# Kernel optimization log

Hardware: AMD Instinct MI355X
Metric: run time of the kernel (lower is better)

## Reference

```python
import jax, jax.numpy as jnp
import numpy as np

SCALE = 1.0 / np.sqrt(64.0)  # module hardcodes 64**0.5, independent of d


def setup_inputs() -> dict:
    key = jax.random.key(0)
    k1, k2 = jax.random.split(key)
    x = jax.random.normal(k1, (8, 2048, 512), dtype=jnp.float32)
    kernel = jax.random.normal(k2, (3, 512, 512), dtype=jnp.float32) * 0.02
    return {"x": x, "kernel": kernel}


def reference(x, kernel):
    # x: [b, s, d]; kernel: [3, d, d]
    q = jnp.einsum('bsd,de->bse', x, kernel[0])
    k = jnp.einsum('bsd,de->bse', x, kernel[1])
    v = jnp.einsum('bsd,de->bse', x, kernel[2])
    scores = jnp.einsum('bqd,bkd->bqk', q, k) * SCALE  # [b, s, s]
    attn = jax.nn.softmax(scores, axis=-1)
    return jnp.einsum('bqk,bkd->bqd', attn, v)
```

## Files before the change

kernel.cpp:

```cpp
#include <hip/hip_runtime.h>


typedef unsigned short u16;
typedef unsigned int u32;

using bf16x8 = __attribute__((ext_vector_type(8))) short;
using f32x4  = __attribute__((ext_vector_type(4))) float;
using u16x4  = __attribute__((ext_vector_type(4))) u16;

__device__ __forceinline__ u16 f2bf(float f) {
  u32 u = __float_as_uint(f);
  u32 r = (u + 0x7FFFu + ((u >> 16) & 1u)) >> 16;
  return (u16)r;
}
__device__ __forceinline__ float bf2f(u16 h) {
  return __uint_as_float(((u32)h) << 16);
}

#define GLL16(src, dst)                                                        \
  __builtin_amdgcn_global_load_lds(                                            \
      (const __attribute__((address_space(1))) void*)(src),                    \
      (__attribute__((address_space(3))) void*)(dst), 16, 0, 0)

template <int K, bool RSUM>
__device__ __forceinline__ void gemm8p_256x128(
    const u16* __restrict__ A0, const u16* __restrict__ B0,
    u16* lds, f32x4 (&acc)[4][4], float* rs)
{
  const int tid = threadIdx.x;
  const int w = tid >> 6, l = tid & 63;
  const int wm = w >> 1, wn = w & 1;
  const int fr = l & 15;
  const int laneChunk = ((l >> 4) ^ ((fr >> 1) & 3)) << 3;
  const int laneA = (wm * 64 + fr) * 32 + laneChunk;
  const int laneB = (wn * 64 + fr) * 32 + laneChunk;
  u16* const ldsA = lds;
  u16* const ldsB = lds + 24576;

  const int chunkS = ((tid & 3) ^ ((tid >> 3) & 3)) << 3;
  const int r0 = tid >> 2;
  const u16* const sA0 = A0 + (size_t)r0 * K + chunkS;
  const u16* const sA1 = A0 + (size_t)(r0 + 128) * K + chunkS;
  const u16* const sB0 = B0 + (size_t)r0 * K + chunkS;
  const int dOf = w * 512;

#define PSTAGE_A(j, slot) do {                                                 \
    u16* d_ = ldsA + (slot) * 8192 + dOf;                                      \
    GLL16(sA0 + (j) * 32, d_);                                                 \
    GLL16(sA1 + (j) * 32, d_ + 4096);                                          \
  } while (0)
#define PSTAGE_B(j, slot) do {                                                 \
    u16* d_ = ldsB + (slot) * 4096 + dOf;                                      \
    GLL16(sB0 + (j) * 32, d_);                                                 \
  } while (0)

  PSTAGE_B(0, 0); PSTAGE_A(0, 0);
  PSTAGE_B(1, 1); PSTAGE_A(1, 1);

  constexpr int NS = K / 32;
  int slot = 0;
  for (int j = 0; j < NS; ++j) {
    const int jn = (j + 2 < NS) ? (j + 2) : (NS - 1);
    int slotn = slot + 2; if (slotn >= 3) slotn -= 3;

    asm volatile("s_waitcnt vmcnt(3)\n\ts_barrier" ::: "memory");

    const u16* const Ab = ldsA + slot * 8192;
    const u16* const Bb = ldsB + slot * 4096;
    bf16x8 a[4], b[4];
#pragma unroll
    for (int i = 0; i < 4; ++i) a[i] = *(const bf16x8*)(Ab + laneA + i * 512);
#pragma unroll
    for (int i = 0; i < 4; ++i) b[i] = *(const bf16x8*)(Bb + laneB + i * 512);
    PSTAGE_B(jn, slotn);
    __builtin_amdgcn_s_setprio(1);
#pragma unroll
    for (int mi = 0; mi < 2; ++mi)
#pragma unroll
      for (int nj = 0; nj < 4; ++nj)
        acc[mi][nj] = __builtin_amdgcn_mfma_f32_16x16x32_bf16(a[mi], b[nj], acc[mi][nj], 0, 0, 0);
    __builtin_amdgcn_s_setprio(0);
    PSTAGE_A(jn, slotn);
    __builtin_amdgcn_s_setprio(1);
#pragma unroll
    for (int mi = 2; mi < 4; ++mi)
#pragma unroll
      for (int nj = 0; nj < 4; ++nj)
        acc[mi][nj] = __builtin_amdgcn_mfma_f32_16x16x32_bf16(a[mi], b[nj], acc[mi][nj], 0, 0, 0);
    __builtin_amdgcn_s_setprio(0);

    if (RSUM) {
#pragma unroll
      for (int i = 0; i < 4; ++i) {
        float s_ = 0.f;
#pragma unroll
        for (int e = 0; e < 8; ++e) s_ += bf2f((u16)a[i][e]);
        rs[i] += s_;
      }
    }

    slot = (slot == 2) ? 0 : slot + 1;
  }
#undef PSTAGE_A
#undef PSTAGE_B
}

template <int K>
__device__ __forceinline__ void gemm8p_256sq_pp(
    const u16* __restrict__ A0, const u16* __restrict__ B0,
    u16* lds, f32x4 (&acc)[8][4])
{
  const int tid = threadIdx.x;
  const int w = tid >> 6, l = tid & 63;
  const int wm = w >> 2, wn = w & 3;
  const int fr = l & 15;
  const int laneChunk = ((l >> 4) ^ ((fr >> 1) & 3)) << 3;
  const int laneA = (wm * 128 + fr) * 32 + laneChunk;
  const int laneB = (wn * 64 + fr) * 32 + laneChunk;
  u16* const ldsA = lds;
  u16* const ldsB = lds + 24576;

  const int chunkS = ((tid & 3) ^ ((tid >> 3) & 3)) << 3;
  const int r0 = tid >> 2;
  const u16* const sA0 = A0 + (size_t)r0 * K + chunkS;
  const u16* const sA1 = A0 + (size_t)(r0 + 128) * K + chunkS;
  const u16* const sB0 = B0 + (size_t)r0 * K + chunkS;
  const u16* const sB1 = B0 + (size_t)(r0 + 128) * K + chunkS;
  const int dOf = w * 512;

#define SSTAGE_A(j, slot) do {                                                 \
    u16* d_ = ldsA + (slot) * 8192 + dOf;                                      \
    GLL16(sA0 + (j) * 32, d_);                                                 \
    GLL16(sA1 + (j) * 32, d_ + 4096);                                          \
  } while (0)
#define SSTAGE_B(j, slot) do {                                                 \
    u16* d_ = ldsB + (slot) * 8192 + dOf;                                      \
    GLL16(sB0 + (j) * 32, d_);                                                 \
    GLL16(sB1 + (j) * 32, d_ + 4096);                                          \
  } while (0)

  constexpr int NS = K / 32;
  bf16x8 bP[4], aP0[4], aP1[4], bQ[4], aQ0[4], aQ1[4];

  SSTAGE_B(0, 0); SSTAGE_A(0, 0);
  SSTAGE_B(1, 1); SSTAGE_A(1, 1);
  SSTAGE_B(2, 2); SSTAGE_A(2, 2);
  asm volatile("s_waitcnt vmcnt(8)\n\ts_barrier" ::: "memory");
#pragma unroll
  for (int i = 0; i < 4; ++i) bP[i]  = *(const bf16x8*)(ldsB + laneB + i * 512);
#pragma unroll
  for (int i = 0; i < 4; ++i) aP0[i] = *(const bf16x8*)(ldsA + laneA + i * 512);
#pragma unroll
  for (int i = 0; i < 4; ++i) aP1[i] = *(const bf16x8*)(ldsA + laneA + (4 + i) * 512);

#define SITER(jj, CB, CA0, CA1, NB, NA0, NA1) do {                             \
    const int js_ = ((jj) + 3 < NS) ? (jj) + 3 : NS - 1;                       \
    const int sS_ = (jj) % 3;                                                  \
    const int sR_ = ((jj) + 1) % 3;                                            \
    asm volatile("s_waitcnt vmcnt(4) lgkmcnt(0)\n\ts_barrier" ::: "memory");   \
    const u16* const Ab_ = ldsA + sR_ * 8192;                                  \
    const u16* const Bb_ = ldsB + sR_ * 8192;                                  \
    _Pragma("unroll")                                                          \
    for (int i = 0; i < 4; ++i) NB[i]  = *(const bf16x8*)(Bb_ + laneB + i * 512); \
    _Pragma("unroll")                                                          \
    for (int i = 0; i < 4; ++i) NA0[i] = *(const bf16x8*)(Ab_ + laneA + i * 512); \
    SSTAGE_A(js_, sS_);                                                        \
    __builtin_amdgcn_s_setprio(1);                                             \
    _Pragma("unroll")                                                          \
    for (int mi = 0; mi < 4; ++mi)                                             \
      _Pragma("unroll")                                                        \
      for (int nj = 0; nj < 4; ++nj)                                           \
        acc[mi][nj] = __builtin_amdgcn_mfma_f32_16x16x32_bf16(                 \
            CA0[mi], CB[nj], acc[mi][nj], 0, 0, 0);                            \
    __builtin_amdgcn_s_setprio(0);                                             \
    _Pragma("unroll")                                                          \
    for (int i = 0; i < 4; ++i) NA1[i] = *(const bf16x8*)(Ab_ + laneA + (4 + i) * 512); \
    SSTAGE_B(js_, sS_);                                                        \
    __builtin_amdgcn_s_setprio(1);                                             \
    _Pragma("unroll")                                                          \
    for (int mi = 0; mi < 4; ++mi)                                             \
      _Pragma("unroll")                                                        \
      for (int nj = 0; nj < 4; ++nj)                                           \
        acc[4 + mi][nj] = __builtin_amdgcn_mfma_f32_16x16x32_bf16(             \
            CA1[mi], CB[nj], acc[4 + mi][nj], 0, 0, 0);                        \
    __builtin_amdgcn_s_setprio(0);                                             \
  } while (0)

  for (int j = 0; j < NS; j += 2) {
    SITER(j, bP, aP0, aP1, bQ, aQ0, aQ1);
    SITER(j + 1, bQ, aQ0, aQ1, bP, aP0, aP1);
  }
#undef SITER
#undef SSTAGE_A
#undef SSTAGE_B
}


__global__ void convert_x_kernel(const float* __restrict__ x, u16* __restrict__ xb) {
  int i = blockIdx.x * 256 + threadIdx.x;
  float4 f = ((const float4*)x)[i];
  u16x4 o = { f2bf(f.x), f2bf(f.y), f2bf(f.z), f2bf(f.w) };
  ((u16x4*)xb)[i] = o;
}

__global__ void convw_kernel(const float* __restrict__ W, u16* __restrict__ wT) {
  __shared__ float tile[32][33];
  const int mtx = blockIdx.z;
  const int e0 = blockIdx.x * 32, d0 = blockIdx.y * 32;
  const int tx = threadIdx.x, ty = threadIdx.y;
  const float* Wm = W + (size_t)mtx * 262144;
#pragma unroll
  for (int i = 0; i < 32; i += 8)
    tile[ty + i][tx] = Wm[(size_t)(d0 + ty + i) * 512 + e0 + tx];
  __syncthreads();
  u16* T = wT + (size_t)mtx * 262144;
#pragma unroll
  for (int i = 0; i < 32; i += 8)
    T[(size_t)(e0 + ty + i) * 512 + d0 + tx] = f2bf(tile[tx][ty + i]);
}

__global__ __launch_bounds__(512, 4) void gemm_qkv128_kernel(
    const u16* __restrict__ xb, const u16* __restrict__ wT,
    u16* __restrict__ qb, u16* __restrict__ kb, u16* __restrict__ vt)
{
  __shared__ __align__(16) u16 lds[36864];
  const int id = blockIdx.x;
  const int xcd = id & 7, t = id >> 3;
  const int n0 = (t % 12) * 128;
  const int m0 = (xcd * 8 + t / 12) * 256;
  f32x4 acc[4][4] = {};
  gemm8p_256x128<512, false>(xb + (size_t)m0 * 512, wT + (size_t)n0 * 512, lds, acc, nullptr);

  const int tid = threadIdx.x, w = tid >> 6, l = tid & 63;
  const int wm = w >> 1, wn = w & 1;
  const int which = n0 >> 9;
  const int eb = (n0 & 511) + wn * 64 + (l & 15);
  const int rb = m0 + wm * 64 + (l >> 4) * 4;
  if (which < 2) {
    u16* dst = which ? kb : qb;
#pragma unroll
    for (int mi = 0; mi < 4; ++mi)
#pragma unroll
      for (int nj = 0; nj < 4; ++nj) {
        const int row = rb + mi * 16;
        const int col = eb + nj * 16;
#pragma unroll
        for (int r = 0; r < 4; ++r)
          dst[(size_t)(row + r) * 512 + col] = f2bf(acc[mi][nj][r]);
      }
  } else {
#pragma unroll
    for (int mi = 0; mi < 4; ++mi)
#pragma unroll
      for (int nj = 0; nj < 4; ++nj) {
        const int s = rb + mi * 16;
        const int b = s >> 11, sl = s & 2047;
        const int e = eb + nj * 16;
        u16x4 pk;
#pragma unroll
        for (int r = 0; r < 4; ++r) pk[r] = f2bf(acc[mi][nj][r]);
        *(u16x4*)(vt + (size_t)b * 1048576 + (size_t)e * 2048 + sl) = pk;
      }
  }
}

__global__ __launch_bounds__(512, 2) void gemm_scores256_kernel(
    const u16* __restrict__ qb, const u16* __restrict__ kb, u16* __restrict__ attn)
{
  __shared__ __align__(16) u16 lds[49152];
  const int id = blockIdx.x;
  const int z = id & 7, t = id >> 3;
  const int n0 = (t & 7) * 256;
  const int m0 = (t >> 3) * 256;
  f32x4 acc[8][4] = {};
  gemm8p_256sq_pp<512>(qb + (size_t)z * 1048576 + (size_t)m0 * 512,
                       kb + (size_t)z * 1048576 + (size_t)n0 * 512, lds, acc);

  const int tid = threadIdx.x, w = tid >> 6, l = tid & 63;
  const int wm = w >> 2, wn = w & 3;
  u16* C = attn + (size_t)z * 4194304;
  const int rb = m0 + wm * 128 + (l >> 4) * 4;
  const int cb = n0 + wn * 64 + (l & 15);
#pragma unroll
  for (int mi = 0; mi < 8; ++mi)
#pragma unroll
    for (int nj = 0; nj < 4; ++nj) {
      const int row = rb + mi * 16;
      const int col = cb + nj * 16;
#pragma unroll
      for (int r = 0; r < 4; ++r)
        C[(size_t)(row + r) * 2048 + col] = f2bf(__expf(acc[mi][nj][r] * 0.125f));
    }
}

__global__ __launch_bounds__(512, 4) void gemm_pv8p_kernel(
    const u16* __restrict__ attn, const u16* __restrict__ vt, float* __restrict__ out)
{
  __shared__ __align__(16) u16 lds[36864];
  __shared__ float rowsumLDS[256];
  const int id = blockIdx.x;
  const int z = id & 7;
  const int j = id >> 3;
  const int n0 = (j & 3) * 128;
  const int m0 = (j >> 2) * 256;
  f32x4 acc[4][4] = {};
  float rs[4] = {0.f, 0.f, 0.f, 0.f};
  gemm8p_256x128<2048, true>(attn + (size_t)z * 4194304 + (size_t)m0 * 2048,
                             vt + (size_t)z * 1048576 + (size_t)n0 * 2048, lds, acc, rs);

  const int tid = threadIdx.x, w = tid >> 6, l = tid & 63;
  const int wm = w >> 1, wn = w & 1;

  __syncthreads();
#pragma unroll
  for (int mi = 0; mi < 4; ++mi) {
    rs[mi] += __shfl_xor(rs[mi], 16);
    rs[mi] += __shfl_xor(rs[mi], 32);
  }
  if ((l >> 4) == 0) {
#pragma unroll
    for (int mi = 0; mi < 4; ++mi)
      rowsumLDS[wm * 64 + mi * 16 + l] = rs[mi];
  }
  __syncthreads();

  float* C = out + (size_t)z * 1048576;
  const int rb = m0 + wm * 64 + (l >> 4) * 4;
  const int cb = n0 + wn * 64 + (l & 15);
#pragma unroll
  for (int mi = 0; mi < 4; ++mi)
#pragma unroll
    for (int r = 0; r < 4; ++r) {
      const float inv = 1.f / rowsumLDS[wm * 64 + mi * 16 + (l >> 4) * 4 + r];
      const int row = rb + mi * 16 + r;
#pragma unroll
      for (int nj = 0; nj < 4; ++nj)
        C[(size_t)row * 512 + cb + nj * 16] = acc[mi][nj][r] * inv;
    }
}

extern "C" void kernel_launch(void* const* d_in, const int* in_sizes, int n_in,
                              void* d_out, int out_size, void* d_ws, size_t ws_size,
                              hipStream_t stream) {
  const float* x = (const float*)d_in[0];
  const float* W = (const float*)d_in[1];
  float* out = (float*)d_out;

  if (ws_size < 117440512) return;
  u16* wsu  = (u16*)d_ws;
  u16* qb   = wsu;
  u16* kb   = qb + 8388608;
  u16* vt   = kb + 8388608;
  u16* attn = vt + 8388608;
  u16* xb   = attn;
  u16* wT   = attn + 8388608;

  convert_x_kernel<<<8192, 256, 0, stream>>>(x, xb);
  convw_kernel<<<dim3(16, 16, 3), dim3(32, 8), 0, stream>>>(W, wT);
  gemm_qkv128_kernel<<<768, 512, 0, stream>>>(xb, wT, qb, kb, vt);
  gemm_scores256_kernel<<<512, 512, 0, stream>>>(qb, kb, attn);
  gemm_pv8p_kernel<<<256, 512, 0, stream>>>(attn, vt, out);
}
```

Before: 132.0 us.

## Register double-buffer GEMM fragments and move softmax rowsum into scores epilogue

The 256x128 GEMM core now prefetches the next k-step's LDS fragments into a second register set while MFMAs run on the current one, with three stages of global loads in flight. When the workspace is large enough, the scores kernel accumulates exp row sums in fp32 and atomically adds them to a global buffer, which convert_x zeroes beforehand. The PV kernel then reads these sums instead of re-summing bf16 attention fragments. This removes per-iteration rowsum ALU work in PV, at the cost of atomics in the scores epilogue, more register pressure, and a fast path that only runs if the workspace exceeds the prior size.

```diff
diff --git a/kernel.cpp b/kernel.cpp
--- a/kernel.cpp
+++ b/kernel.cpp
@@ -23,7 +23,7 @@
       (__attribute__((address_space(3))) void*)(dst), 16, 0, 0)
 
 template <int K, bool RSUM>
-__device__ __forceinline__ void gemm8p_256x128(
+__device__ __forceinline__ void gemm128_pp(
     const u16* __restrict__ A0, const u16* __restrict__ B0,
     u16* lds, f32x4 (&acc)[4][4], float* rs)
 {
@@ -54,53 +54,63 @@
     GLL16(sB0 + (j) * 32, d_);                                                 \
   } while (0)
 
+  constexpr int NS = K / 32;
+  bf16x8 aP[4], bP[4], aQ[4], bQ[4];
+
   PSTAGE_B(0, 0); PSTAGE_A(0, 0);
   PSTAGE_B(1, 1); PSTAGE_A(1, 1);
-
-  constexpr int NS = K / 32;
-  int slot = 0;
-  for (int j = 0; j < NS; ++j) {
-    const int jn = (j + 2 < NS) ? (j + 2) : (NS - 1);
-    int slotn = slot + 2; if (slotn >= 3) slotn -= 3;
-
-    asm volatile("s_waitcnt vmcnt(3)\n\ts_barrier" ::: "memory");
-
-    const u16* const Ab = ldsA + slot * 8192;
-    const u16* const Bb = ldsB + slot * 4096;
-    bf16x8 a[4], b[4];
-#pragma unroll
-    for (int i = 0; i < 4; ++i) a[i] = *(const bf16x8*)(Ab + laneA + i * 512);
-#pragma unroll
-    for (int i = 0; i < 4; ++i) b[i] = *(const bf16x8*)(Bb + laneB + i * 512);
-    PSTAGE_B(jn, slotn);
-    __builtin_amdgcn_s_setprio(1);
-#pragma unroll
-    for (int mi = 0; mi < 2; ++mi)
-#pragma unroll
-      for (int nj = 0; nj < 4; ++nj)
-        acc[mi][nj] = __builtin_amdgcn_mfma_f32_16x16x32_bf16(a[mi], b[nj], acc[mi][nj], 0, 0, 0);
-    __builtin_amdgcn_s_setprio(0);
-    PSTAGE_A(jn, slotn);
-    __builtin_amdgcn_s_setprio(1);
-#pragma unroll
-    for (int mi = 2; mi < 4; ++mi)
-#pragma unroll
-      for (int nj = 0; nj < 4; ++nj)
-        acc[mi][nj] = __builtin_amdgcn_mfma_f32_16x16x32_bf16(a[mi], b[nj], acc[mi][nj], 0, 0, 0);
-    __builtin_amdgcn_s_setprio(0);
-
-    if (RSUM) {
-#pragma unroll
-      for (int i = 0; i < 4; ++i) {
-        float s_ = 0.f;
-#pragma unroll
-        for (int e = 0; e < 8; ++e) s_ += bf2f((u16)a[i][e]);
-        rs[i] += s_;
-      }
-    }
-
-    slot = (slot == 2) ? 0 : slot + 1;
+  PSTAGE_B(2, 2); PSTAGE_A(2, 2);
+  asm volatile("s_waitcnt vmcnt(6)\n\ts_barrier" ::: "memory");
+#pragma unroll
+  for (int i = 0; i < 4; ++i) aP[i] = *(const bf16x8*)(ldsA + laneA + i * 512);
+#pragma unroll
+  for (int i = 0; i < 4; ++i) bP[i] = *(const bf16x8*)(ldsB + laneB + i * 512);
+
+#define KITER(jj, CA, CB, NA, NB) do {                                         \
+    const int js_ = ((jj) + 3 < NS) ? (jj) + 3 : NS - 1;                       \
+    const int sS_ = (jj) % 3;                                                  \
+    const int sR_ = ((jj) + 1) % 3;                                            \
+    asm volatile("s_waitcnt vmcnt(3) lgkmcnt(0)\n\ts_barrier" ::: "memory");   \
+    const u16* const Ab_ = ldsA + sR_ * 8192;                                  \
+    const u16* const Bb_ = ldsB + sR_ * 4096;                                  \
+    _Pragma("unroll")                                                          \
+    for (int i = 0; i < 4; ++i) NB[i] = *(const bf16x8*)(Bb_ + laneB + i * 512); \
+    _Pragma("unroll")                                                          \
+    for (int i = 0; i < 4; ++i) NA[i] = *(const bf16x8*)(Ab_ + laneA + i * 512); \
+    PSTAGE_B(js_, sS_);                                                        \
+    __builtin_amdgcn_s_setprio(1);                                             \
+    _Pragma("unroll")                                                          \
+    for (int mi = 0; mi < 2; ++mi)                                             \
+      _Pragma("unroll")                                                        \
+      for (int nj = 0; nj < 4; ++nj)                                           \
+        acc[mi][nj] = __builtin_amdgcn_mfma_f32_16x16x32_bf16(                 \
+            CA[mi], CB[nj], acc[mi][nj], 0, 0, 0);                             \
+    __builtin_amdgcn_s_setprio(0);                                             \
+    PSTAGE_A(js_, sS_);                                                        \
+    __builtin_amdgcn_s_setprio(1);                                             \
+    _Pragma("unroll")                                                          \
+    for (int mi = 2; mi < 4; ++mi)                                             \
+      _Pragma("unroll")                                                        \
+      for (int nj = 0; nj < 4; ++nj)                                           \
+        acc[mi][nj] = __builtin_amdgcn_mfma_f32_16x16x32_bf16(                 \
+            CA[mi], CB[nj], acc[mi][nj], 0, 0, 0);                             \
+    __builtin_amdgcn_s_setprio(0);                                             \
+    if (RSUM) {                                                                \
+      _Pragma("unroll")                                                        \
+      for (int i = 0; i < 4; ++i) {                                            \
+        float s_ = 0.f;                                                        \
+        _Pragma("unroll")                                                      \
+        for (int e = 0; e < 8; ++e) s_ += bf2f((u16)CA[i][e]);                 \
+        rs[i] += s_;                                                           \
+      }                                                                        \
+    }                                                                          \
+  } while (0)
+
+  for (int j = 0; j < NS; j += 2) {
+    KITER(j, aP, bP, aQ, bQ);
+    KITER(j + 1, aQ, bQ, aP, bP);
   }
+#undef KITER
 #undef PSTAGE_A
 #undef PSTAGE_B
 }
@@ -196,11 +206,14 @@
 }
 
 
-__global__ void convert_x_kernel(const float* __restrict__ x, u16* __restrict__ xb) {
+__global__ void convert_x_kernel(const float* __restrict__ x, u16* __restrict__ xb,
+                                 float* __restrict__ rsum) {
   int i = blockIdx.x * 256 + threadIdx.x;
   float4 f = ((const float4*)x)[i];
   u16x4 o = { f2bf(f.x), f2bf(f.y), f2bf(f.z), f2bf(f.w) };
   ((u16x4*)xb)[i] = o;
+  if (rsum != nullptr && blockIdx.x < 64)
+    rsum[blockIdx.x * 256 + threadIdx.x] = 0.f;
 }
 
 __global__ void convw_kernel(const float* __restrict__ W, u16* __restrict__ wT) {
@@ -229,7 +242,7 @@
   const int n0 = (t % 12) * 128;
   const int m0 = (xcd * 8 + t / 12) * 256;
   f32x4 acc[4][4] = {};
-  gemm8p_256x128<512, false>(xb + (size_t)m0 * 512, wT + (size_t)n0 * 512, lds, acc, nullptr);
+  gemm128_pp<512, false>(xb + (size_t)m0 * 512, wT + (size_t)n0 * 512, lds, acc, nullptr);
 
   const int tid = threadIdx.x, w = tid >> 6, l = tid & 63;
   const int wm = w >> 1, wn = w & 1;
@@ -265,7 +278,8 @@
 }
 
 __global__ __launch_bounds__(512, 2) void gemm_scores256_kernel(
-    const u16* __restrict__ qb, const u16* __restrict__ kb, u16* __restrict__ attn)
+    const u16* __restrict__ qb, const u16* __restrict__ kb,
+    u16* __restrict__ attn, float* __restrict__ rsum)
 {
   __shared__ __align__(16) u16 lds[49152];
   const int id = blockIdx.x;
@@ -281,6 +295,12 @@
   u16* C = attn + (size_t)z * 4194304;
   const int rb = m0 + wm * 128 + (l >> 4) * 4;
   const int cb = n0 + wn * 64 + (l & 15);
+  float rp[8][4];
+#pragma unroll
+  for (int mi = 0; mi < 8; ++mi)
+#pragma unroll
+    for (int r = 0; r < 4; ++r) rp[mi][r] = 0.f;
+
 #pragma unroll
   for (int mi = 0; mi < 8; ++mi)
 #pragma unroll
@@ -288,13 +308,33 @@
       const int row = rb + mi * 16;
       const int col = cb + nj * 16;
 #pragma unroll
-      for (int r = 0; r < 4; ++r)
-        C[(size_t)(row + r) * 2048 + col] = f2bf(__expf(acc[mi][nj][r] * 0.125f));
+      for (int r = 0; r < 4; ++r) {
+        const float e = __expf(acc[mi][nj][r] * 0.125f);
+        C[(size_t)(row + r) * 2048 + col] = f2bf(e);
+        rp[mi][r] += e;
+      }
     }
-}
-
+
+  if (rsum != nullptr) {
+    float* rz = rsum + (size_t)z * 2048;
+#pragma unroll
+    for (int mi = 0; mi < 8; ++mi)
+#pragma unroll
+      for (int r = 0; r < 4; ++r) {
+        float v = rp[mi][r];
+        v += __shfl_xor(v, 1);
+        v += __shfl_xor(v, 2);
+        v += __shfl_xor(v, 4);
+        v += __shfl_xor(v, 8);
+        if ((l & 15) == 0) atomicAdd(&rz[rb + mi * 16 + r], v);
+      }
+  }
+}
+
+template <bool FAST>
 __global__ __launch_bounds__(512, 4) void gemm_pv8p_kernel(
-    const u16* __restrict__ attn, const u16* __restrict__ vt, float* __restrict__ out)
+    const u16* __restrict__ attn, const u16* __restrict__ vt,
+    const float* __restrict__ rsum, float* __restrict__ out)
 {
   __shared__ __align__(16) u16 lds[36864];
   __shared__ float rowsumLDS[256];
@@ -305,38 +345,51 @@
   const int m0 = (j >> 2) * 256;
   f32x4 acc[4][4] = {};
   float rs[4] = {0.f, 0.f, 0.f, 0.f};
-  gemm8p_256x128<2048, true>(attn + (size_t)z * 4194304 + (size_t)m0 * 2048,
-                             vt + (size_t)z * 1048576 + (size_t)n0 * 2048, lds, acc, rs);
+  gemm128_pp<2048, !FAST>(attn + (size_t)z * 4194304 + (size_t)m0 * 2048,
+                          vt + (size_t)z * 1048576 + (size_t)n0 * 2048, lds, acc, rs);
 
   const int tid = threadIdx.x, w = tid >> 6, l = tid & 63;
   const int wm = w >> 1, wn = w & 1;
-
-  __syncthreads();
-#pragma unroll
-  for (int mi = 0; mi < 4; ++mi) {
-    rs[mi] += __shfl_xor(rs[mi], 16);
-    rs[mi] += __shfl_xor(rs[mi], 32);
-  }
-  if ((l >> 4) == 0) {
-#pragma unroll
-    for (int mi = 0; mi < 4; ++mi)
-      rowsumLDS[wm * 64 + mi * 16 + l] = rs[mi];
-  }
-  __syncthreads();
-
-  float* C = out + (size_t)z * 1048576;
   const int rb = m0 + wm * 64 + (l >> 4) * 4;
   const int cb = n0 + wn * 64 + (l & 15);
-#pragma unroll
-  for (int mi = 0; mi < 4; ++mi)
-#pragma unroll
-    for (int r = 0; r < 4; ++r) {
-      const float inv = 1.f / rowsumLDS[wm * 64 + mi * 16 + (l >> 4) * 4 + r];
-      const int row = rb + mi * 16 + r;
-#pragma unroll
-      for (int nj = 0; nj < 4; ++nj)
-        C[(size_t)row * 512 + cb + nj * 16] = acc[mi][nj][r] * inv;
+  float* C = out + (size_t)z * 1048576;
+
+  if (FAST) {
+    const float* rz = rsum + (size_t)z * 2048;
+#pragma unroll
+    for (int mi = 0; mi < 4; ++mi)
+#pragma unroll
+      for (int r = 0; r < 4; ++r) {
+        const float inv = 1.f / rz[rb + mi * 16 + r];
+        const int row = rb + mi * 16 + r;
+#pragma unroll
+        for (int nj = 0; nj < 4; ++nj)
+          C[(size_t)row * 512 + cb + nj * 16] = acc[mi][nj][r] * inv;
+      }
+  } else {
+    __syncthreads();
+#pragma unroll
+    for (int mi = 0; mi < 4; ++mi) {
+      rs[mi] += __shfl_xor(rs[mi], 16);
+      rs[mi] += __shfl_xor(rs[mi], 32);
     }
+    if ((l >> 4) == 0) {
+#pragma unroll
+      for (int mi = 0; mi < 4; ++mi)
+        rowsumLDS[wm * 64 + mi * 16 + l] = rs[mi];
+    }
+    __syncthreads();
+#pragma unroll
+    for (int mi = 0; mi < 4; ++mi)
+#pragma unroll
+      for (int r = 0; r < 4; ++r) {
+        const float inv = 1.f / rowsumLDS[wm * 64 + mi * 16 + (l >> 4) * 4 + r];
+        const int row = rb + mi * 16 + r;
+#pragma unroll
+        for (int nj = 0; nj < 4; ++nj)
+          C[(size_t)row * 512 + cb + nj * 16] = acc[mi][nj][r] * inv;
+      }
+  }
 }
 
 extern "C" void kernel_launch(void* const* d_in, const int* in_sizes, int n_in,
@@ -355,9 +408,15 @@
   u16* xb   = attn;
   u16* wT   = attn + 8388608;
 
-  convert_x_kernel<<<8192, 256, 0, stream>>>(x, xb);
+  const bool fast = ws_size >= 117440512 + 65536;
+  float* rsum = fast ? (float*)(wsu + 58720256) : nullptr;
+
+  convert_x_kernel<<<8192, 256, 0, stream>>>(x, xb, rsum);
   convw_kernel<<<dim3(16, 16, 3), dim3(32, 8), 0, stream>>>(W, wT);
   gemm_qkv128_kernel<<<768, 512, 0, stream>>>(xb, wT, qb, kb, vt);
-  gemm_scores256_kernel<<<512, 512, 0, stream>>>(qb, kb, attn);
-  gemm_pv8p_kernel<<<256, 512, 0, stream>>>(attn, vt, out);
-}
+  gemm_scores256_kernel<<<512, 512, 0, stream>>>(qb, kb, attn, rsum);
+  if (fast)
+    gemm_pv8p_kernel<true><<<256, 512, 0, stream>>>(attn, vt, rsum, out);
+  else
+    gemm_pv8p_kernel<false><<<256, 512, 0, stream>>>(attn, vt, nullptr, out);
+}
```

New measurement: 273.1 us. 2.07x slower.

## Split PV row-sum into separate kernel and use ping-pong pipelined PV GEMM

Applied to the files above, without the earlier changes.

Moves the softmax row-sum out of the PV GEMM inner loop into a standalone rowsum kernel, so the PV GEMM can run a lighter ping-pong register-buffered, triple-staged pipeline with priority hints around the MFMA blocks. This takes the per-iteration bf16-to-float row-sum work out of the GEMM. In exchange the attention matrix is read twice and there is an extra launch. The fast path runs only when the workspace has 64KB extra beyond the old requirement, otherwise it falls back to the old kernel.

```diff
diff --git a/kernel.cpp b/kernel.cpp
--- a/kernel.cpp
+++ b/kernel.cpp
@@ -106,6 +106,90 @@
 }
 
 template <int K>
+__device__ __forceinline__ void gemm128_pp(
+    const u16* __restrict__ A0, const u16* __restrict__ B0,
+    u16* lds, f32x4 (&acc)[4][4])
+{
+  const int tid = threadIdx.x;
+  const int w = tid >> 6, l = tid & 63;
+  const int wm = w >> 1, wn = w & 1;
+  const int fr = l & 15;
+  const int laneChunk = ((l >> 4) ^ ((fr >> 1) & 3)) << 3;
+  const int laneA = (wm * 64 + fr) * 32 + laneChunk;
+  const int laneB = (wn * 64 + fr) * 32 + laneChunk;
+  u16* const ldsA = lds;
+  u16* const ldsB = lds + 24576;
+
+  const int chunkS = ((tid & 3) ^ ((tid >> 3) & 3)) << 3;
+  const int r0 = tid >> 2;
+  const u16* const sA0 = A0 + (size_t)r0 * K + chunkS;
+  const u16* const sA1 = A0 + (size_t)(r0 + 128) * K + chunkS;
+  const u16* const sB0 = B0 + (size_t)r0 * K + chunkS;
+  const int dOf = w * 512;
+
+#define PSTAGE_A(j, slot) do {                                                 \
+    u16* d_ = ldsA + (slot) * 8192 + dOf;                                      \
+    GLL16(sA0 + (j) * 32, d_);                                                 \
+    GLL16(sA1 + (j) * 32, d_ + 4096);                                          \
+  } while (0)
+#define PSTAGE_B(j, slot) do {                                                 \
+    u16* d_ = ldsB + (slot) * 4096 + dOf;                                      \
+    GLL16(sB0 + (j) * 32, d_);                                                 \
+  } while (0)
+
+  constexpr int NS = K / 32;
+  bf16x8 aP[4], bP[4], aQ[4], bQ[4];
+
+  PSTAGE_B(0, 0); PSTAGE_A(0, 0);
+  PSTAGE_B(1, 1); PSTAGE_A(1, 1);
+  PSTAGE_B(2, 2); PSTAGE_A(2, 2);
+  asm volatile("s_waitcnt vmcnt(6)\n\ts_barrier" ::: "memory");
+#pragma unroll
+  for (int i = 0; i < 4; ++i) aP[i] = *(const bf16x8*)(ldsA + laneA + i * 512);
+#pragma unroll
+  for (int i = 0; i < 4; ++i) bP[i] = *(const bf16x8*)(ldsB + laneB + i * 512);
+
+#define KITER(jj, CA, CB, NA, NB) do {                                         \
+    const int js_ = ((jj) + 3 < NS) ? (jj) + 3 : NS - 1;                       \
+    const int sS_ = (jj) % 3;                                                  \
+    const int sR_ = ((jj) + 1) % 3;                                            \
+    asm volatile("s_waitcnt vmcnt(3) lgkmcnt(0)\n\ts_barrier" ::: "memory");   \
+    const u16* const Ab_ = ldsA + sR_ * 8192;                                  \
+    const u16* const Bb_ = ldsB + sR_ * 4096;                                  \
+    _Pragma("unroll")                                                          \
+    for (int i = 0; i < 4; ++i) NB[i] = *(const bf16x8*)(Bb_ + laneB + i * 512); \
+    _Pragma("unroll")                                                          \
+    for (int i = 0; i < 4; ++i) NA[i] = *(const bf16x8*)(Ab_ + laneA + i * 512); \
+    PSTAGE_B(js_, sS_);                                                        \
+    __builtin_amdgcn_s_setprio(1);                                             \
+    _Pragma("unroll")                                                          \
+    for (int mi = 0; mi < 2; ++mi)                                             \
+      _Pragma("unroll")                                                        \
+      for (int nj = 0; nj < 4; ++nj)                                           \
+        acc[mi][nj] = __builtin_amdgcn_mfma_f32_16x16x32_bf16(                 \
+            CA[mi], CB[nj], acc[mi][nj], 0, 0, 0);                             \
+    __builtin_amdgcn_s_setprio(0);                                             \
+    PSTAGE_A(js_, sS_);                                                        \
+    __builtin_amdgcn_s_setprio(1);                                             \
+    _Pragma("unroll")                                                          \
+    for (int mi = 2; mi < 4; ++mi)                                             \
+      _Pragma("unroll")                                                        \
+      for (int nj = 0; nj < 4; ++nj)                                           \
+        acc[mi][nj] = __builtin_amdgcn_mfma_f32_16x16x32_bf16(                 \
+            CA[mi], CB[nj], acc[mi][nj], 0, 0, 0);                             \
+    __builtin_amdgcn_s_setprio(0);                                             \
+  } while (0)
+
+  for (int j = 0; j < NS; j += 2) {
+    KITER(j, aP, bP, aQ, bQ);
+    KITER(j + 1, aQ, bQ, aP, bP);
+  }
+#undef KITER
+#undef PSTAGE_A
+#undef PSTAGE_B
+}
+
+template <int K>
 __device__ __forceinline__ void gemm8p_256sq_pp(
     const u16* __restrict__ A0, const u16* __restrict__ B0,
     u16* lds, f32x4 (&acc)[8][4])
@@ -293,8 +377,59 @@
     }
 }
 
-__global__ __launch_bounds__(512, 4) void gemm_pv8p_kernel(
-    const u16* __restrict__ attn, const u16* __restrict__ vt, float* __restrict__ out)
+__global__ __launch_bounds__(256) void rowsum_kernel(
+    const u16* __restrict__ attn, float* __restrict__ rsum)
+{
+  const int row = blockIdx.x * 4 + (threadIdx.x >> 6);
+  const int l = threadIdx.x & 63;
+  const u16* p = attn + (size_t)row * 2048;
+  float s = 0.f;
+#pragma unroll
+  for (int c = 0; c < 4; ++c) {
+    uint4 u = *(const uint4*)(p + (c * 64 + l) * 8);
+    const u16* us = (const u16*)&u;
+#pragma unroll
+    for (int i = 0; i < 8; ++i) s += bf2f(us[i]);
+  }
+  for (int off = 32; off >= 1; off >>= 1) s += __shfl_xor(s, off);
+  if (l == 0) rsum[row] = s;
+}
+
+__global__ __launch_bounds__(512, 2) void gemm_pv_pp_kernel(
+    const u16* __restrict__ attn, const u16* __restrict__ vt,
+    const float* __restrict__ rsum, float* __restrict__ out)
+{
+  __shared__ __align__(16) u16 lds[36864];
+  const int id = blockIdx.x;
+  const int z = id & 7;
+  const int j = id >> 3;
+  const int n0 = (j & 3) * 128;
+  const int m0 = (j >> 2) * 256;
+  f32x4 acc[4][4] = {};
+  gemm128_pp<2048>(attn + (size_t)z * 4194304 + (size_t)m0 * 2048,
+                   vt + (size_t)z * 1048576 + (size_t)n0 * 2048, lds, acc);
+
+  const int tid = threadIdx.x, w = tid >> 6, l = tid & 63;
+  const int wm = w >> 1, wn = w & 1;
+  const int rb = m0 + wm * 64 + (l >> 4) * 4;
+  const int cb = n0 + wn * 64 + (l & 15);
+  float* C = out + (size_t)z * 1048576;
+  const float* rz = rsum + (size_t)z * 2048;
+#pragma unroll
+  for (int mi = 0; mi < 4; ++mi)
+#pragma unroll
+    for (int r = 0; r < 4; ++r) {
+      const float inv = 1.f / rz[rb + mi * 16 + r];
+      const int row = rb + mi * 16 + r;
+#pragma unroll
+      for (int nj = 0; nj < 4; ++nj)
+        C[(size_t)row * 512 + cb + nj * 16] = acc[mi][nj][r] * inv;
+    }
+}
+
+__global__ __launch_bounds__(512, 4) void gemm_pv_fb_kernel(
+    const u16* __restrict__ attn, const u16* __restrict__ vt,
+    float* __restrict__ out)
 {
   __shared__ __align__(16) u16 lds[36864];
   __shared__ float rowsumLDS[256];
@@ -310,7 +445,6 @@
 
   const int tid = threadIdx.x, w = tid >> 6, l = tid & 63;
   const int wm = w >> 1, wn = w & 1;
-
   __syncthreads();
 #pragma unroll
   for (int mi = 0; mi < 4; ++mi) {
@@ -355,9 +489,17 @@
   u16* xb   = attn;
   u16* wT   = attn + 8388608;
 
+  const bool fast = ws_size >= 117440512 + 65536;
+  float* rsum = fast ? (float*)(wsu + 58720256) : nullptr;
+
   convert_x_kernel<<<8192, 256, 0, stream>>>(x, xb);
   convw_kernel<<<dim3(16, 16, 3), dim3(32, 8), 0, stream>>>(W, wT);
   gemm_qkv128_kernel<<<768, 512, 0, stream>>>(xb, wT, qb, kb, vt);
   gemm_scores256_kernel<<<512, 512, 0, stream>>>(qb, kb, attn);
-  gemm_pv8p_kernel<<<256, 512, 0, stream>>>(attn, vt, out);
-}
+  if (fast) {
+    rowsum_kernel<<<4096, 256, 0, stream>>>(attn, rsum);
+    gemm_pv_pp_kernel<<<256, 512, 0, stream>>>(attn, vt, rsum, out);
+  } else {
+    gemm_pv_fb_kernel<<<256, 512, 0, stream>>>(attn, vt, out);
+  }
+}
```

Measured after the change: 135.1 us. 1.02x slower.
